# Kernel optimization log

Measured on AMD Instinct MI355X. Metric: run time of the kernel, lower is better.

## Reference

```python
import jax, jax.numpy as jnp
import numpy as np
from math import sqrt

EMBED = 1024
HEADS = 16

def setup_inputs() -> dict:
    key = jax.random.key(0)
    k1, k2, k3, k4, k5 = jax.random.split(key, 5)
    x = jax.random.normal(k1, (2, 2048, EMBED), dtype=jnp.float32)
    s = 1.0 / sqrt(EMBED)
    W_qkv = jax.random.normal(k2, (EMBED, 3 * EMBED), dtype=jnp.float32) * s
    b_qkv = jax.random.normal(k3, (3 * EMBED,), dtype=jnp.float32) * 0.01
    W_out = jax.random.normal(k4, (EMBED, EMBED), dtype=jnp.float32) * s
    b_out = jax.random.normal(k5, (EMBED,), dtype=jnp.float32) * 0.01
    return {"x": x, "W_qkv": W_qkv, "b_qkv": b_qkv, "W_out": W_out, "b_out": b_out}

def reference(x, W_qkv, b_qkv, W_out, b_out) -> jnp.ndarray:
    B, N, E = x.shape
    H = HEADS
    d = E // H
    qkv = x @ W_qkv + b_qkv                       # [B, N, 3E]
    q, k, v = jnp.split(qkv, 3, axis=2)
    # b n (h e) -> b n h e
    q = q.reshape(B, N, H, d)
    k = k.reshape(B, N, H, d)
    v = v.reshape(B, N, H, d)
    energy = jnp.einsum('bqhe,bkhe->bqhk', q, k)  # [B, N, H, N]
    # NOTE: original divides AFTER softmax, by sqrt(embed_size) (not head dim)
    attn = jax.nn.softmax(energy, axis=-1) / sqrt(E)
    out = jnp.einsum('bihv,bvhd->bihd', attn, v)  # [B, N, H, d]
    out = out.reshape(B, N, E)
    # dropout in eval mode -> identity
    return out @ W_out + b_out
```

## Files before the change

### kernel.cpp

```cpp
#include <hip/hip_runtime.h>
#include <hip/hip_bf16.h>

#define EMBED 1024
#define HEADS 16
#define HDIM 64
#define BATCH 2
#define SEQ 2048
#define ROWS (BATCH*SEQ)
#define QKV_N (3*EMBED)

typedef __attribute__((ext_vector_type(8))) short bf16x8;
typedef __attribute__((ext_vector_type(4))) float f32x4;
typedef __attribute__((ext_vector_type(16))) float f32x16;
typedef __hip_bfloat16 bf16;

__device__ inline f32x4 mfma16(bf16x8 a, bf16x8 b, f32x4 c) {
  return __builtin_amdgcn_mfma_f32_16x16x32_bf16(a, b, c, 0, 0, 0);
}
__device__ inline f32x16 mfma32(bf16x8 a, bf16x8 b, f32x16 c) {
  return __builtin_amdgcn_mfma_f32_32x32x16_bf16(a, b, c, 0, 0, 0);
}
__device__ inline unsigned pk2(float a, float b) {
  union { unsigned u; unsigned short s[2]; } r;
  union { bf16 h; unsigned short v; } ca, cb;
  ca.h = __float2bfloat16(a); cb.h = __float2bfloat16(b);
  r.s[0] = ca.v; r.s[1] = cb.v;
  return r.u;
}

__device__ inline void gload_lds16(const bf16* g, bf16* l) {
  __builtin_amdgcn_global_load_lds(
      (const __attribute__((address_space(1))) unsigned int*)g,
      (__attribute__((address_space(3))) unsigned int*)l, 16, 0, 0);
}

__global__ void cast_x_kernel(const float* __restrict__ in, bf16* __restrict__ out, int n4) {
  int i = blockIdx.x * blockDim.x + threadIdx.x;
  if (i >= n4) return;
  float4 v = reinterpret_cast<const float4*>(in)[i];
  union { ushort4 u; bf16 b[4]; } cv;
  cv.b[0] = __float2bfloat16(v.x);
  cv.b[1] = __float2bfloat16(v.y);
  cv.b[2] = __float2bfloat16(v.z);
  cv.b[3] = __float2bfloat16(v.w);
  reinterpret_cast<ushort4*>(out)[i] = cv.u;
}

__global__ void transpose_cast_kernel(const float* __restrict__ in, bf16* __restrict__ out,
                                      int R, int C) {
  __shared__ float tile[32][33];
  int c0 = blockIdx.x * 32, r0 = blockIdx.y * 32;
  int tx = threadIdx.x, ty = threadIdx.y;
  #pragma unroll
  for (int i = ty; i < 32; i += 8)
    tile[i][tx] = in[(size_t)(r0 + i) * C + c0 + tx];
  __syncthreads();
  #pragma unroll
  for (int i = ty; i < 32; i += 8)
    out[(size_t)(c0 + i) * R + r0 + tx] = __float2bfloat16(tile[tx][i]);
}

__global__ void transpose_v_kernel(const bf16* __restrict__ qkv, bf16* __restrict__ vT) {
  __shared__ bf16 tile[32][33];
  int bh = blockIdx.z, b = bh >> 4, h = bh & 15;
  int t0 = blockIdx.x * 32, d0 = blockIdx.y * 32;
  int tx = threadIdx.x, ty = threadIdx.y;
  #pragma unroll
  for (int i = ty; i < 32; i += 8)
    tile[i][tx] = qkv[(size_t)(b*SEQ + t0 + i) * QKV_N + 2*EMBED + h*HDIM + d0 + tx];
  __syncthreads();
  #pragma unroll
  for (int i = ty; i < 32; i += 8)
    vT[((size_t)bh*HDIM + d0 + i) * SEQ + t0 + tx] = tile[tx][i];
}

template<int OUT_FP32>
__global__ __launch_bounds__(256) void gemm_bias_kernel(
    const bf16* __restrict__ A, const bf16* __restrict__ Bt,
    const float* __restrict__ bias, void* __restrict__ Cout,
    int M, int N, int K) {
  __shared__ __align__(16) bf16 Ash[128*32];
  __shared__ __align__(16) bf16 Bsh[128*32];
  const int m0 = blockIdx.y * 128, n0 = blockIdx.x * 128;
  const int tid = threadIdx.x, wave = tid >> 6, lane = tid & 63;
  const int wm = wave >> 1, wn = wave & 1;
  const int ll = lane & 15, lg = lane >> 4;
  f32x4 acc[4][4] = {};

  for (int k0 = 0; k0 < K; k0 += 32) {
    #pragma unroll
    for (int c = 0; c < 2; c++) {
      int li = (wave + c*4) * 64 + lane;
      gload_lds16(A + (size_t)(m0 + (li >> 2)) * K + k0 + (li & 3) * 8,
                  Ash + (size_t)(wave + c*4) * 512);
      gload_lds16(Bt + (size_t)(n0 + (li >> 2)) * K + k0 + (li & 3) * 8,
                  Bsh + (size_t)(wave + c*4) * 512);
    }
    __syncthreads();
    bf16x8 af[4], bfr[4];
    #pragma unroll
    for (int mi = 0; mi < 4; mi++)
      af[mi] = *reinterpret_cast<const bf16x8*>(&Ash[(wm*64 + mi*16 + ll)*32 + lg*8]);
    #pragma unroll
    for (int ni = 0; ni < 4; ni++)
      bfr[ni] = *reinterpret_cast<const bf16x8*>(&Bsh[(wn*64 + ni*16 + ll)*32 + lg*8]);
    #pragma unroll
    for (int mi = 0; mi < 4; mi++)
      #pragma unroll
      for (int ni = 0; ni < 4; ni++)
        acc[mi][ni] = mfma16(af[mi], bfr[ni], acc[mi][ni]);
    __syncthreads();
  }

  #pragma unroll
  for (int mi = 0; mi < 4; mi++) {
    #pragma unroll
    for (int ni = 0; ni < 4; ni++) {
      int col = n0 + wn*64 + ni*16 + ll;
      float bs = bias[col];
      #pragma unroll
      for (int r = 0; r < 4; r++) {
        int row = m0 + wm*64 + mi*16 + lg*4 + r;
        float v = acc[mi][ni][r] + bs;
        if (OUT_FP32) reinterpret_cast<float*>(Cout)[(size_t)row * N + col] = v;
        else          reinterpret_cast<bf16*>(Cout)[(size_t)row * N + col] = __float2bfloat16(v);
      }
    }
  }
}

__global__ __launch_bounds__(512) void flash_attn9_kernel(
    const bf16* __restrict__ qkv, const bf16* __restrict__ vT, bf16* __restrict__ O) {
  const int lid = blockIdx.y * gridDim.x + blockIdx.x;
  const int wid = (lid & 7) * 64 + (lid >> 3);
  const int qt = wid & 15, bh = wid >> 4;
  const int b = bh >> 4, h = bh & 15;
  const int lane = threadIdx.x & 63, wv = threadIdx.x >> 6;
  const int w_q = wv >> 1, w_s = wv & 1;
  const int q32 = lane & 31, hi = lane >> 5;
  const int qrow = qt * 128 + w_q * 32 + q32;
  const float L2E = 1.44269504088896f;

  __shared__ __align__(16) char smem[65536];
  float* cb_o  = (float*)smem;
  float* cb_ml = (float*)(smem + 32768);

  const bf16* qp = qkv + (size_t)(b*SEQ + qrow) * QKV_N + h*HDIM + hi*8;
  bf16x8 qf[4];
  #pragma unroll
  for (int ks = 0; ks < 4; ks++)
    qf[ks] = *reinterpret_cast<const bf16x8*>(qp + ks*16);

  float m_run = -1e30f, l_run = 0.0f;
  f32x16 oa[2] = {};

  const bf16* kb = qkv + (size_t)(b*SEQ)*QKV_N + EMBED + h*HDIM;
  const bf16* vb = vT + (size_t)bh * HDIM * SEQ;

  const int srow = (lane >> 3);
  const int schunk = (lane & 7) ^ srow;
  const int r0 = w_q * 16;
  const int kt0 = w_s * (SEQ/2);

  auto STAGE = [&](int t, int buf) {
    const int kt = kt0 + t*64;
    bf16* Kd = (bf16*)(smem + buf*32768) + w_s*4096;
    bf16* Vd = (bf16*)(smem + buf*32768 + 16384) + w_s*4096;
    #pragma unroll
    for (int i = 0; i < 2; i++) {
      const int row = r0 + i*8 + srow;
      gload_lds16(kb + (size_t)(kt + row)*QKV_N + schunk*8, Kd + (r0 + i*8)*64);
      gload_lds16(vb + (size_t)row*SEQ + kt + schunk*8,     Vd + (r0 + i*8)*64);
    }
  };

  STAGE(0, 0);
  for (int t = 0; t < 16; t++) {
    const int cur = t & 1;
    if (t < 15) {
      STAGE(t+1, cur^1);
      asm volatile("s_waitcnt vmcnt(4)" ::: "memory");
    } else {
      asm volatile("s_waitcnt vmcnt(0)" ::: "memory");
    }
    __builtin_amdgcn_s_barrier();
    __builtin_amdgcn_sched_barrier(0);

    const bf16* Kl = (const bf16*)(smem + cur*32768) + w_s*4096;
    const bf16* Vl = (const bf16*)(smem + cur*32768 + 16384) + w_s*4096;

    bf16x8 kf[8], vf[8];
    #pragma unroll
    for (int hh = 0; hh < 2; hh++) {
      const int tk = hh*32 + q32;
      #pragma unroll
      for (int ks = 0; ks < 4; ks++)
        kf[hh*4+ks] = *reinterpret_cast<const bf16x8*>(
            Kl + tk*64 + (((ks*2+hi) ^ (tk&7)) << 3));
    }
    #pragma unroll
    for (int dh = 0; dh < 2; dh++) {
      const int dr = dh*32 + q32;
      #pragma unroll
      for (int ks = 0; ks < 4; ks++)
        vf[ks*2+dh] = *reinterpret_cast<const bf16x8*>(
            Vl + dr*64 + (((ks*2+hi) ^ (dr&7)) << 3));
    }

    f32x16 s[2] = {};
    #pragma unroll
    for (int ks = 0; ks < 4; ks++) {
      s[0] = mfma32(kf[ks],   qf[ks], s[0]);
      s[1] = mfma32(kf[4+ks], qf[ks], s[1]);
    }

    float t16[16];
    #pragma unroll
    for (int r = 0; r < 16; r++) t16[r] = fmaxf(s[0][r], s[1][r]);
    #pragma unroll
    for (int r = 0; r < 8; r++) t16[r] = fmaxf(t16[r], t16[r+8]);
    #pragma unroll
    for (int r = 0; r < 4; r++) t16[r] = fmaxf(t16[r], t16[r+4]);
    float mx = fmaxf(fmaxf(t16[0], t16[1]), fmaxf(t16[2], t16[3]));
    mx = fmaxf(mx, __shfl_xor(mx, 32));

    if (!__all(mx <= m_run + 8.0f)) {
      const float mnew = fmaxf(m_run, mx);
      const float sc = exp2f((m_run - mnew) * L2E);
      m_run = mnew;
      l_run *= sc;
      #pragma unroll
      for (int dh = 0; dh < 2; dh++)
        #pragma unroll
        for (int r = 0; r < 16; r++) oa[dh][r] *= sc;
    }
    const float nm = -m_run * L2E;

    float p[32];
    #pragma unroll
    for (int hh = 0; hh < 2; hh++)
      #pragma unroll
      for (int r = 0; r < 16; r++)
        p[hh*16+r] = __builtin_amdgcn_exp2f(fmaf(s[hh][r], L2E, nm));

    float a16[16];
    #pragma unroll
    for (int r = 0; r < 16; r++) a16[r] = p[r] + p[r+16];
    #pragma unroll
    for (int r = 0; r < 8; r++) a16[r] += a16[r+8];
    #pragma unroll
    for (int r = 0; r < 4; r++) a16[r] += a16[r+4];
    float rs = (a16[0] + a16[1]) + (a16[2] + a16[3]);
    rs += __shfl_xor(rs, 32);
    l_run += rs;

    union PWU { unsigned w[4]; bf16x8 v; } pw[4];
    #pragma unroll
    for (int hh = 0; hh < 2; hh++) {
      #pragma unroll
      for (int k2 = 0; k2 < 2; k2++) {
        const int b0 = hh*16 + k2*8;
        unsigned WA = pk2(p[b0+0], p[b0+1]);
        unsigned WB = pk2(p[b0+2], p[b0+3]);
        unsigned WC = pk2(p[b0+4], p[b0+5]);
        unsigned WD = pk2(p[b0+6], p[b0+7]);
        asm volatile("v_permlane32_swap_b32 %0, %1" : "+v"(WA), "+v"(WC));
        asm volatile("v_permlane32_swap_b32 %0, %1" : "+v"(WB), "+v"(WD));
        const int ks = hh*2 + k2;
        pw[ks].w[0] = WA;
        pw[ks].w[1] = WB;
        pw[ks].w[2] = WC;
        pw[ks].w[3] = WD;
      }
    }

    #pragma unroll
    for (int ks = 0; ks < 4; ks++) {
      oa[0] = mfma32(vf[ks*2+0], pw[ks].v, oa[0]);
      oa[1] = mfma32(vf[ks*2+1], pw[ks].v, oa[1]);
    }
    __builtin_amdgcn_s_barrier();
    __builtin_amdgcn_sched_barrier(0);
  }

  if (w_s == 1) {
    cb_ml[(w_q*2+0)*64 + lane] = m_run;
    cb_ml[(w_q*2+1)*64 + lane] = l_run;
    #pragma unroll
    for (int dh = 0; dh < 2; dh++)
      #pragma unroll
      for (int r = 0; r < 16; r++)
        cb_o[(w_q*32 + dh*16+r)*64 + lane] = oa[dh][r];
  }
  __syncthreads();
  if (w_s == 0) {
    const float m1 = cb_ml[(w_q*2+0)*64 + lane];
    const float l1 = cb_ml[(w_q*2+1)*64 + lane];
    const float M  = fmaxf(m_run, m1);
    const float a0 = exp2f((m_run - M) * L2E);
    const float a1 = exp2f((m1   - M) * L2E);
    const float inv = 1.0f / ((l_run * a0 + l1 * a1) * 32.0f);
    bf16* orow = O + (size_t)(b*SEQ + qrow) * EMBED + h*HDIM;
    #pragma unroll
    for (int dh = 0; dh < 2; dh++) {
      #pragma unroll
      for (int tt = 0; tt < 4; tt++) {
        union { ushort4 u; unsigned short s4[4]; } st;
        #pragma unroll
        for (int r = 0; r < 4; r++) {
          float v = (oa[dh][tt*4+r] * a0 + cb_o[(w_q*32 + dh*16+tt*4+r)*64 + lane] * a1) * inv;
          union { bf16 hh2; unsigned short v2; } c;
          c.hh2 = __float2bfloat16(v);
          st.s4[r] = c.v2;
        }
        *reinterpret_cast<ushort4*>(orow + dh*32 + tt*8 + hi*4) = st.u;
      }
    }
  }
}

extern "C" void kernel_launch(void* const* d_in, const int* in_sizes, int n_in,
                              void* d_out, int out_size, void* d_ws, size_t ws_size,
                              hipStream_t stream) {
  const float* x     = (const float*)d_in[0];
  const float* W_qkv = (const float*)d_in[1];
  const float* b_qkv = (const float*)d_in[2];
  const float* W_out = (const float*)d_in[3];
  const float* b_out = (const float*)d_in[4];
  float* out = (float*)d_out;

  char* ws = (char*)d_ws;
  bf16* qkv   = (bf16*)(ws);
  bf16* vTb   = (bf16*)(ws + 25165824);
  bf16* Obuf  = (bf16*)(ws + 33554432);
  bf16* xb    = (bf16*)(ws + 41943040);
  bf16* WqkvT = (bf16*)(ws + 50331648);
  bf16* WoutT = (bf16*)(ws + 56623104);

  cast_x_kernel<<<(ROWS*EMBED/4 + 255)/256, 256, 0, stream>>>(x, xb, ROWS*EMBED/4);
  transpose_cast_kernel<<<dim3(QKV_N/32, EMBED/32), dim3(32,8), 0, stream>>>(W_qkv, WqkvT, EMBED, QKV_N);
  transpose_cast_kernel<<<dim3(EMBED/32, EMBED/32), dim3(32,8), 0, stream>>>(W_out, WoutT, EMBED, EMBED);
  gemm_bias_kernel<0><<<dim3(QKV_N/128, ROWS/128), 256, 0, stream>>>(xb, WqkvT, b_qkv, qkv, ROWS, QKV_N, EMBED);
  transpose_v_kernel<<<dim3(SEQ/32, HDIM/32, BATCH*HEADS), dim3(32,8), 0, stream>>>(qkv, vTb);
  flash_attn9_kernel<<<dim3(16, BATCH*HEADS), 512, 0, stream>>>(qkv, vTb, Obuf);
  gemm_bias_kernel<1><<<dim3(EMBED/128, ROWS/128), 256, 0, stream>>>(Obuf, WoutT, b_out, out, ROWS, EMBED, EMBED);
}
```

Measured before the change: 143.8 us.

## Double-buffer GEMM LDS loads and restructure attention to single-split with direct V loads

The GEMM kernel now double-buffers its A/B LDS tiles so the next K-slice loads while MFMAs run on the current one, replacing the two __syncthreads per step with raw barriers. The attention kernel drops the two-way key split across waves and the LDS combine step, using 256-thread blocks that walk the full sequence. It stages only K through LDS, reads V fragments directly from global memory, and adds s_setprio around the MFMA sections. This aims to cut LDS footprint for higher occupancy and remove the cross-wave merge, but relies on the cache to serve uncoalesced global V reads and halves the per-block parallelism.

```diff
diff --git a/kernel.cpp b/kernel.cpp
--- a/kernel.cpp
+++ b/kernel.cpp
@@ -79,37 +79,54 @@
     const bf16* __restrict__ A, const bf16* __restrict__ Bt,
     const float* __restrict__ bias, void* __restrict__ Cout,
     int M, int N, int K) {
-  __shared__ __align__(16) bf16 Ash[128*32];
-  __shared__ __align__(16) bf16 Bsh[128*32];
+  __shared__ __align__(16) bf16 Ash[2][128*32];
+  __shared__ __align__(16) bf16 Bsh[2][128*32];
   const int m0 = blockIdx.y * 128, n0 = blockIdx.x * 128;
   const int tid = threadIdx.x, wave = tid >> 6, lane = tid & 63;
   const int wm = wave >> 1, wn = wave & 1;
   const int ll = lane & 15, lg = lane >> 4;
   f32x4 acc[4][4] = {};
 
-  for (int k0 = 0; k0 < K; k0 += 32) {
+  auto STAGE = [&](int t, int buf) {
+    const int k0 = t * 32;
     #pragma unroll
     for (int c = 0; c < 2; c++) {
       int li = (wave + c*4) * 64 + lane;
       gload_lds16(A + (size_t)(m0 + (li >> 2)) * K + k0 + (li & 3) * 8,
-                  Ash + (size_t)(wave + c*4) * 512);
+                  &Ash[buf][(size_t)(wave + c*4) * 512]);
       gload_lds16(Bt + (size_t)(n0 + (li >> 2)) * K + k0 + (li & 3) * 8,
-                  Bsh + (size_t)(wave + c*4) * 512);
-    }
-    __syncthreads();
+                  &Bsh[buf][(size_t)(wave + c*4) * 512]);
+    }
+  };
+
+  const int NT = K / 32;
+  STAGE(0, 0);
+  for (int t = 0; t < NT; t++) {
+    const int cur = t & 1;
+    if (t < NT - 1) {
+      STAGE(t + 1, cur ^ 1);
+      asm volatile("s_waitcnt vmcnt(4)" ::: "memory");
+    } else {
+      asm volatile("s_waitcnt vmcnt(0)" ::: "memory");
+    }
+    __builtin_amdgcn_s_barrier();
+    __builtin_amdgcn_sched_barrier(0);
+
     bf16x8 af[4], bfr[4];
     #pragma unroll
     for (int mi = 0; mi < 4; mi++)
-      af[mi] = *reinterpret_cast<const bf16x8*>(&Ash[(wm*64 + mi*16 + ll)*32 + lg*8]);
+      af[mi] = *reinterpret_cast<const bf16x8*>(&Ash[cur][(wm*64 + mi*16 + ll)*32 + lg*8]);
     #pragma unroll
     for (int ni = 0; ni < 4; ni++)
-      bfr[ni] = *reinterpret_cast<const bf16x8*>(&Bsh[(wn*64 + ni*16 + ll)*32 + lg*8]);
+      bfr[ni] = *reinterpret_cast<const bf16x8*>(&Bsh[cur][(wn*64 + ni*16 + ll)*32 + lg*8]);
     #pragma unroll
     for (int mi = 0; mi < 4; mi++)
       #pragma unroll
       for (int ni = 0; ni < 4; ni++)
         acc[mi][ni] = mfma16(af[mi], bfr[ni], acc[mi][ni]);
-    __syncthreads();
+
+    __builtin_amdgcn_s_barrier();
+    __builtin_amdgcn_sched_barrier(0);
   }
 
   #pragma unroll
@@ -129,21 +146,18 @@
   }
 }
 
-__global__ __launch_bounds__(512) void flash_attn9_kernel(
+__global__ __launch_bounds__(256, 4) void flash_attn10_kernel(
     const bf16* __restrict__ qkv, const bf16* __restrict__ vT, bf16* __restrict__ O) {
   const int lid = blockIdx.y * gridDim.x + blockIdx.x;
   const int wid = (lid & 7) * 64 + (lid >> 3);
   const int qt = wid & 15, bh = wid >> 4;
   const int b = bh >> 4, h = bh & 15;
   const int lane = threadIdx.x & 63, wv = threadIdx.x >> 6;
-  const int w_q = wv >> 1, w_s = wv & 1;
   const int q32 = lane & 31, hi = lane >> 5;
-  const int qrow = qt * 128 + w_q * 32 + q32;
+  const int qrow = qt * 128 + wv * 32 + q32;
   const float L2E = 1.44269504088896f;
 
-  __shared__ __align__(16) char smem[65536];
-  float* cb_o  = (float*)smem;
-  float* cb_ml = (float*)(smem + 32768);
+  __shared__ __align__(16) char smem[16384];
 
   const bf16* qp = qkv + (size_t)(b*SEQ + qrow) * QKV_N + h*HDIM + hi*8;
   bf16x8 qf[4];
@@ -159,37 +173,29 @@
 
   const int srow = (lane >> 3);
   const int schunk = (lane & 7) ^ srow;
-  const int r0 = w_q * 16;
-  const int kt0 = w_s * (SEQ/2);
+  const int r0 = wv * 16;
 
   auto STAGE = [&](int t, int buf) {
-    const int kt = kt0 + t*64;
-    bf16* Kd = (bf16*)(smem + buf*32768) + w_s*4096;
-    bf16* Vd = (bf16*)(smem + buf*32768 + 16384) + w_s*4096;
+    const int kt = t * 64;
+    bf16* Kd = (bf16*)(smem + buf*8192);
     #pragma unroll
     for (int i = 0; i < 2; i++) {
       const int row = r0 + i*8 + srow;
       gload_lds16(kb + (size_t)(kt + row)*QKV_N + schunk*8, Kd + (r0 + i*8)*64);
-      gload_lds16(vb + (size_t)row*SEQ + kt + schunk*8,     Vd + (r0 + i*8)*64);
     }
   };
 
   STAGE(0, 0);
-  for (int t = 0; t < 16; t++) {
+  for (int t = 0; t < 32; t++) {
     const int cur = t & 1;
-    if (t < 15) {
-      STAGE(t+1, cur^1);
-      asm volatile("s_waitcnt vmcnt(4)" ::: "memory");
-    } else {
-      asm volatile("s_waitcnt vmcnt(0)" ::: "memory");
-    }
+    const int kt = t * 64;
+    asm volatile("s_waitcnt vmcnt(0)" ::: "memory");
     __builtin_amdgcn_s_barrier();
     __builtin_amdgcn_sched_barrier(0);
 
-    const bf16* Kl = (const bf16*)(smem + cur*32768) + w_s*4096;
-    const bf16* Vl = (const bf16*)(smem + cur*32768 + 16384) + w_s*4096;
-
-    bf16x8 kf[8], vf[8];
+    const bf16* Kl = (const bf16*)(smem + cur*8192);
+
+    bf16x8 kf[8];
     #pragma unroll
     for (int hh = 0; hh < 2; hh++) {
       const int tk = hh*32 + q32;
@@ -198,21 +204,29 @@
         kf[hh*4+ks] = *reinterpret_cast<const bf16x8*>(
             Kl + tk*64 + (((ks*2+hi) ^ (tk&7)) << 3));
     }
-    #pragma unroll
-    for (int dh = 0; dh < 2; dh++) {
-      const int dr = dh*32 + q32;
-      #pragma unroll
-      for (int ks = 0; ks < 4; ks++)
-        vf[ks*2+dh] = *reinterpret_cast<const bf16x8*>(
-            Vl + dr*64 + (((ks*2+hi) ^ (dr&7)) << 3));
-    }
 
     f32x16 s[2] = {};
+    __builtin_amdgcn_s_setprio(1);
     #pragma unroll
     for (int ks = 0; ks < 4; ks++) {
       s[0] = mfma32(kf[ks],   qf[ks], s[0]);
       s[1] = mfma32(kf[4+ks], qf[ks], s[1]);
     }
+    __builtin_amdgcn_s_setprio(0);
+
+    bf16x8 vf[8];
+    #pragma unroll
+    for (int dh = 0; dh < 2; dh++) {
+      const int dr = dh*32 + q32;
+      #pragma unroll
+      for (int ks = 0; ks < 4; ks++)
+        vf[ks*2+dh] = *reinterpret_cast<const bf16x8*>(
+            vb + (size_t)dr*SEQ + kt + (ks*2+hi)*8);
+    }
+    __builtin_amdgcn_sched_barrier(0);
+
+    if (t < 31) STAGE(t+1, cur^1);
+    __builtin_amdgcn_sched_barrier(0);
 
     float t16[16];
     #pragma unroll
@@ -274,47 +288,33 @@
       }
     }
 
+    __builtin_amdgcn_s_setprio(1);
     #pragma unroll
     for (int ks = 0; ks < 4; ks++) {
       oa[0] = mfma32(vf[ks*2+0], pw[ks].v, oa[0]);
       oa[1] = mfma32(vf[ks*2+1], pw[ks].v, oa[1]);
     }
+    __builtin_amdgcn_s_setprio(0);
+
     __builtin_amdgcn_s_barrier();
     __builtin_amdgcn_sched_barrier(0);
   }
 
-  if (w_s == 1) {
-    cb_ml[(w_q*2+0)*64 + lane] = m_run;
-    cb_ml[(w_q*2+1)*64 + lane] = l_run;
-    #pragma unroll
-    for (int dh = 0; dh < 2; dh++)
-      #pragma unroll
-      for (int r = 0; r < 16; r++)
-        cb_o[(w_q*32 + dh*16+r)*64 + lane] = oa[dh][r];
-  }
-  __syncthreads();
-  if (w_s == 0) {
-    const float m1 = cb_ml[(w_q*2+0)*64 + lane];
-    const float l1 = cb_ml[(w_q*2+1)*64 + lane];
-    const float M  = fmaxf(m_run, m1);
-    const float a0 = exp2f((m_run - M) * L2E);
-    const float a1 = exp2f((m1   - M) * L2E);
-    const float inv = 1.0f / ((l_run * a0 + l1 * a1) * 32.0f);
-    bf16* orow = O + (size_t)(b*SEQ + qrow) * EMBED + h*HDIM;
-    #pragma unroll
-    for (int dh = 0; dh < 2; dh++) {
-      #pragma unroll
-      for (int tt = 0; tt < 4; tt++) {
-        union { ushort4 u; unsigned short s4[4]; } st;
-        #pragma unroll
-        for (int r = 0; r < 4; r++) {
-          float v = (oa[dh][tt*4+r] * a0 + cb_o[(w_q*32 + dh*16+tt*4+r)*64 + lane] * a1) * inv;
-          union { bf16 hh2; unsigned short v2; } c;
-          c.hh2 = __float2bfloat16(v);
-          st.s4[r] = c.v2;
-        }
-        *reinterpret_cast<ushort4*>(orow + dh*32 + tt*8 + hi*4) = st.u;
+  const float inv = 1.0f / (l_run * 32.0f);
+  bf16* orow = O + (size_t)(b*SEQ + qrow) * EMBED + h*HDIM;
+  #pragma unroll
+  for (int dh = 0; dh < 2; dh++) {
+    #pragma unroll
+    for (int tt = 0; tt < 4; tt++) {
+      union { ushort4 u; unsigned short s4[4]; } st;
+      #pragma unroll
+      for (int r = 0; r < 4; r++) {
+        float v = oa[dh][tt*4+r] * inv;
+        union { bf16 hh2; unsigned short v2; } c;
+        c.hh2 = __float2bfloat16(v);
+        st.s4[r] = c.v2;
       }
+      *reinterpret_cast<ushort4*>(orow + dh*32 + tt*8 + hi*4) = st.u;
     }
   }
 }
@@ -342,6 +342,6 @@
   transpose_cast_kernel<<<dim3(EMBED/32, EMBED/32), dim3(32,8), 0, stream>>>(W_out, WoutT, EMBED, EMBED);
   gemm_bias_kernel<0><<<dim3(QKV_N/128, ROWS/128), 256, 0, stream>>>(xb, WqkvT, b_qkv, qkv, ROWS, QKV_N, EMBED);
   transpose_v_kernel<<<dim3(SEQ/32, HDIM/32, BATCH*HEADS), dim3(32,8), 0, stream>>>(qkv, vTb);
-  flash_attn9_kernel<<<dim3(16, BATCH*HEADS), 512, 0, stream>>>(qkv, vTb, Obuf);
+  flash_attn10_kernel<<<dim3(16, BATCH*HEADS), 256, 0, stream>>>(qkv, vTb, Obuf);
   gemm_bias_kernel<1><<<dim3(EMBED/128, ROWS/128), 256, 0, stream>>>(Obuf, WoutT, b_out, out, ROWS, EMBED, EMBED);
 }
```

Result: slower. 210.6 us (+46.5%).
